# Kernel optimization log

Measured on AMD Instinct MI355X. Metric: run time of the kernel, lower is better.

## Reference

```python
import jax, jax.numpy as jnp
import numpy as np

N, K, D, H, DK, DV, E = 20000, 20, 128, 4, 32, 32, 128
HID = 4 * D


def _ln(x, g, b, eps=1e-5):
    m = x.mean(-1, keepdims=True)
    v = ((x - m) ** 2).mean(-1, keepdims=True)
    return (x - m) / jnp.sqrt(v + eps) * g + b


def setup_inputs() -> dict:
    key = jax.random.key(0)
    ks = jax.random.split(key, 24)
    inp = {
        "node_h_src": jax.random.normal(ks[0], (N, K, D), jnp.float32),
        "t": jax.random.uniform(ks[1], (N, K), jnp.float32),
        "t_now": jnp.ones((1,), jnp.float32),
        "edge_feat": jax.random.normal(ks[2], (N, K, E), jnp.float32),
        # time-encoding params (as in __init__)
        "basis_freq": jnp.asarray(1.0 / 10 ** np.linspace(0, 9, D), jnp.float32),
        "phase": jnp.zeros((D,), jnp.float32),
        # edge_fc
        "edge_fc_w": jax.random.normal(ks[3], (E, D), jnp.float32) * 0.05,
        "edge_fc_b": jnp.zeros((D,), jnp.float32),
        # QKV projections (stored as [in, out])
        "w_qs": jax.random.normal(ks[4], (D, H * DK), jnp.float32) * np.sqrt(2.0 / (D + DK)),
        "w_ks": jax.random.normal(ks[5], (D, H * DK), jnp.float32) * np.sqrt(2.0 / (D + DK)),
        "w_vs": jax.random.normal(ks[6], (D, H * DV), jnp.float32) * np.sqrt(2.0 / (D + DV)),
        "w_qs_src": jax.random.normal(ks[7], (D, H * DK), jnp.float32) * np.sqrt(2.0 / (D + DK)),
        # attn output fc
        "attn_fc_w": jax.random.normal(ks[8], (H * DV, D), jnp.float32) * 0.05,
        "attn_fc_b": jnp.zeros((D,), jnp.float32),
        "attn_ln_g": jnp.ones((D,), jnp.float32),
        "attn_ln_b": jnp.zeros((D,), jnp.float32),
        # positionwise FFN (Conv1d kernel 1 == linear)
        "ffn_w1": jax.random.normal(ks[9], (D, HID), jnp.float32) * 0.05,
        "ffn_b1": jnp.zeros((HID,), jnp.float32),
        "ffn_w2": jax.random.normal(ks[10], (HID, D), jnp.float32) * 0.05,
        "ffn_b2": jnp.zeros((D,), jnp.float32),
        "ffn_ln_g": jnp.ones((D,), jnp.float32),
        "ffn_ln_b": jnp.zeros((D,), jnp.float32),
        # fuse + output norm
        "fea2node_w": jax.random.normal(ks[11], (2 * D, D), jnp.float32) * 0.05,
        "fea2node_b": jnp.zeros((D,), jnp.float32),
        "out_ln_g": jnp.ones((D,), jnp.float32),
        "out_ln_b": jnp.zeros((D,), jnp.float32),
    }
    return inp


def reference(node_h_src, t, t_now, edge_feat, basis_freq, phase,
              edge_fc_w, edge_fc_b, w_qs, w_ks, w_vs, w_qs_src,
              attn_fc_w, attn_fc_b, attn_ln_g, attn_ln_b,
              ffn_w1, ffn_b1, ffn_w2, ffn_b2, ffn_ln_g, ffn_ln_b,
              fea2node_w, fea2node_b, out_ln_g, out_ln_b):
    gelu = lambda x: jax.nn.gelu(x, approximate=False)
    # message: temporal encoding + edge feature fusion
    t_enc = jnp.cos((t_now - t)[..., None] * basis_freq + phase)          # [N,K,D]
    z = node_h_src + gelu(edge_feat @ edge_fc_w + edge_fc_b) + t_enc      # [N,K,D]
    q = z @ w_qs                                                          # [N,K,H*DK]
    k = z @ w_ks
    v = z @ w_vs
    # reduce: self message replaces last slot. NOTE: original code uses
    # self_q for q, k AND v (w_ks_src/w_vs_src unused) -- reproduced faithfully.
    self_q = (z[:, -1, :] @ w_qs_src)[:, None, :]                         # [N,1,H*DK]
    q = jnp.concatenate([q[:, :-1, :], self_q], axis=1)
    k = jnp.concatenate([k[:, :-1, :], self_q], axis=1)
    v = jnp.concatenate([v[:, :-1, :], self_q], axis=1)
    qh = q.reshape(N, K, H, DK)
    kh = k.reshape(N, K, H, DK)
    vh = v.reshape(N, K, H, DV)
    attn = jnp.einsum("nqhd,nkhd->nhqk", qh, kh) / jnp.sqrt(jnp.float32(DK))
    attn = jax.nn.softmax(attn, axis=-1)
    out = jnp.einsum("nhqk,nkhd->nqhd", attn, vh).reshape(N, K, H * DV)
    out = out @ attn_fc_w + attn_fc_b
    x = _ln(out + z, attn_ln_g, attn_ln_b)                                # [N,K,D]
    # positionwise FFN with residual + LN
    ffn = jax.nn.relu(x @ ffn_w1 + ffn_b1) @ ffn_w2 + ffn_b2
    x = _ln(ffn + x, ffn_ln_g, ffn_ln_b)
    # fuse self slot with mean of neighbor slots
    neighborhood = x[:, :-1, :].mean(axis=1)                              # [N,D]
    fused = jnp.concatenate([x[:, -1, :], neighborhood], axis=-1)         # [N,2D]
    node_h = _ln(gelu(fused @ fea2node_w + fea2node_b) + node_h_src[:, -1, :],
                 out_ln_g, out_ln_b)
    return node_h
```

## Files before the change

kernel.cpp:

```cpp
#include <hip/hip_runtime.h>
#include <hip/hip_bf16.h>

#define N_NODES 20000
#define KK 20
#define DD 128
#define HH 4
#define DKK 32
#define EE 128
#define HIDD 512
#define RTOT (N_NODES * KK)

using bf16 = __hip_bfloat16;

typedef short s16x8 __attribute__((ext_vector_type(8)));
typedef float f32x4 __attribute__((ext_vector_type(4)));

__device__ __forceinline__ float geluf(float x) {
    return 0.5f * x * (1.0f + erff(x * 0.70710678118654752f));
}

__device__ __forceinline__ float wave_sum(float v) {
#pragma unroll
    for (int o = 32; o > 0; o >>= 1) v += __shfl_down(v, o);
    return __shfl(v, 0);
}

__global__ __launch_bounds__(256)
void k0_conv(const float* __restrict__ w1, const float* __restrict__ w2,
             bf16* __restrict__ w1t, bf16* __restrict__ w2t)
{
    const int id = blockIdx.x * 256 + threadIdx.x;
    if (id < HIDD * DD) {
        const int n = id / DD, k = id % DD;
        w1t[id] = __float2bfloat16(w1[k * HIDD + n]);
    } else {
        const int j = id - HIDD * DD;
        const int n = j / HIDD, k = j % HIDD;
        w2t[j] = __float2bfloat16(w2[k * DD + n]);
    }
}

__global__ __launch_bounds__(256)
void k0b_conv(const float* __restrict__ wq, const float* __restrict__ wk,
              const float* __restrict__ wv, const float* __restrict__ wqs,
              const float* __restrict__ afw, const float* __restrict__ ew,
              bf16* __restrict__ aw)
{
    const int id = blockIdx.x * 256 + threadIdx.x;
    const int m = id >> 14;
    const int r = id & 16383;
    const int n = r >> 7, k = r & 127;
    const float* src = (m == 0) ? wq : (m == 1) ? wk : (m == 2) ? wv
                     : (m == 3) ? wqs : (m == 4) ? afw : ew;
    aw[id] = __float2bfloat16(src[k * DD + n]);
}

__global__ __launch_bounds__(256)
void k1_msg(const float* __restrict__ nhs, const float* __restrict__ t,
            const float* __restrict__ t_now, const float* __restrict__ ef,
            const float* __restrict__ freq, const float* __restrict__ phase,
            const bf16* __restrict__ ewt, const float* __restrict__ eb,
            bf16* __restrict__ z)
{
    __shared__ bf16  efs[32][136];
    __shared__ float gs[32][132];
    __shared__ float ts[32];

    const int tid  = threadIdx.x;
    const int wv   = tid >> 6;
    const int lane = tid & 63;
    const int col  = lane & 15;
    const int quad = lane >> 4;
    const size_t base = (size_t)blockIdx.x * 32 * DD;

    {
        const float4* src = (const float4*)(ef + base);
#pragma unroll
        for (int it = 0; it < 4; it++) {
            const int i = tid + it * 256;
            const int r = i >> 5, c = (i & 31) * 4;
            const float4 v = src[i];
            bf16 tmp[4] = { __float2bfloat16(v.x), __float2bfloat16(v.y),
                            __float2bfloat16(v.z), __float2bfloat16(v.w) };
            *(uint2*)&efs[r][c] = *(const uint2*)tmp;
        }
    }
    if (tid < 32) ts[tid] = t[blockIdx.x * 32 + tid];
    __syncthreads();

    {
        f32x4 acc[2][2];
#pragma unroll
        for (int mt = 0; mt < 2; mt++)
#pragma unroll
            for (int nt = 0; nt < 2; nt++) acc[mt][nt] = (f32x4){0.f, 0.f, 0.f, 0.f};

#pragma unroll
        for (int kk = 0; kk < 4; kk++) {
            const int k0 = kk * 32 + quad * 8;
            const s16x8 a0 = *(const s16x8*)&efs[col][k0];
            const s16x8 a1 = *(const s16x8*)&efs[16 + col][k0];
#pragma unroll
            for (int nt = 0; nt < 2; nt++) {
                const int n = wv * 32 + nt * 16 + col;
                const s16x8 b = *(const s16x8*)&ewt[n * DD + k0];
                acc[0][nt] = __builtin_amdgcn_mfma_f32_16x16x32_bf16(a0, b, acc[0][nt], 0, 0, 0);
                acc[1][nt] = __builtin_amdgcn_mfma_f32_16x16x32_bf16(a1, b, acc[1][nt], 0, 0, 0);
            }
        }

#pragma unroll
        for (int mt = 0; mt < 2; mt++)
#pragma unroll
            for (int nt = 0; nt < 2; nt++) {
                const int n = wv * 32 + nt * 16 + col;
                const float bias = eb[n];
#pragma unroll
                for (int r = 0; r < 4; r++) {
                    const int row = mt * 16 + quad * 4 + r;
                    gs[row][n] = geluf(acc[mt][nt][r] + bias);
                }
            }
    }
    __syncthreads();

    {
        const float tn = t_now[0];
        const float4* nsrc = (const float4*)(nhs + base);
#pragma unroll
        for (int it = 0; it < 4; it++) {
            const int i = tid + it * 256;
            const int r = i >> 5, c = (i & 31) * 4;
            const float4 h  = nsrc[i];
            const float4 fq = *(const float4*)&freq[c];
            const float4 ph = *(const float4*)&phase[c];
            const float dt  = tn - ts[r];
            const float o0 = h.x + gs[r][c + 0] + __cosf(dt * fq.x + ph.x);
            const float o1 = h.y + gs[r][c + 1] + __cosf(dt * fq.y + ph.y);
            const float o2 = h.z + gs[r][c + 2] + __cosf(dt * fq.z + ph.z);
            const float o3 = h.w + gs[r][c + 3] + __cosf(dt * fq.w + ph.w);
            bf16 o[4] = { __float2bfloat16(o0), __float2bfloat16(o1),
                          __float2bfloat16(o2), __float2bfloat16(o3) };
            *(uint2*)&z[base + r * DD + c] = *(const uint2*)o;
        }
    }
}

__global__ __launch_bounds__(256, 4)
void k2_attn(bf16* __restrict__ zx, const bf16* __restrict__ aw,
             const float* __restrict__ afb,
             const float* __restrict__ lng, const float* __restrict__ lnb)
{
    __shared__ __align__(16) char smem[36352];
    bf16  (*zs)[136]    = (bf16  (*)[136])(smem);
    bf16  (*qb)[136]    = (bf16  (*)[136])(smem + 8704);
    bf16  (*kb)[136]    = (bf16  (*)[136])(smem + 17408);
    bf16  (*vT)[40]     = (bf16  (*)[40]) (smem + 26112);
    bf16  (*Pm)[32][40] = (bf16  (*)[32][40])(smem + 8704);
    bf16  (*obf)[136]   = (bf16  (*)[136])(smem + 8704);
    float (*us)[132]    = (float (*)[132])(smem + 8704);

    const int t    = threadIdx.x;
    const int wv4  = t >> 6;
    const int lane = t & 63;
    const int col  = lane & 15;
    const int quad = lane >> 4;
    const int node = blockIdx.x;
    bf16* zrow = zx + node * KK * DD;

    const uint4 z4 = make_uint4(0u, 0u, 0u, 0u);

    {
        const uint4* src = (const uint4*)zrow;
        for (int i = t; i < 320; i += 256) {
            const int r = i >> 4, c = (i & 15) * 8;
            *(uint4*)&zs[r][c] = src[i];
        }
        for (int i = t; i < 204; i += 256) {
            const int r = 20 + i / 17, c = (i % 17) * 8;
            *(uint4*)&zs[r][c] = z4;
        }
    }
    __syncthreads();

    {
        const bf16* Wm = aw + wv4 * (DD * DD);
        f32x4 acc[2][8];
#pragma unroll
        for (int mt = 0; mt < 2; mt++)
#pragma unroll
            for (int nt = 0; nt < 8; nt++) acc[mt][nt] = (f32x4){0.f, 0.f, 0.f, 0.f};

#pragma unroll
        for (int kk = 0; kk < 4; kk++) {
            const int k0 = kk * 32 + quad * 8;
            const s16x8 a0 = *(const s16x8*)&zs[col][k0];
            const s16x8 a1 = *(const s16x8*)&zs[16 + col][k0];
#pragma unroll
            for (int nt = 0; nt < 8; nt++) {
                const s16x8 b = *(const s16x8*)&Wm[(nt * 16 + col) * DD + k0];
                acc[0][nt] = __builtin_amdgcn_mfma_f32_16x16x32_bf16(a0, b, acc[0][nt], 0, 0, 0);
                acc[1][nt] = __builtin_amdgcn_mfma_f32_16x16x32_bf16(a1, b, acc[1][nt], 0, 0, 0);
            }
        }

        if (wv4 < 2) {
            bf16 (*dst)[136] = (wv4 == 0) ? qb : kb;
#pragma unroll
            for (int mt = 0; mt < 2; mt++)
#pragma unroll
                for (int nt = 0; nt < 8; nt++)
#pragma unroll
                    for (int r = 0; r < 4; r++) {
                        const int row = mt * 16 + quad * 4 + r;
                        if (row >= 19) continue;
                        dst[row][nt * 16 + col] = __float2bfloat16(acc[mt][nt][r]);
                    }
        } else if (wv4 == 2) {
#pragma unroll
            for (int mt = 0; mt < 2; mt++)
#pragma unroll
                for (int nt = 0; nt < 8; nt++)
#pragma unroll
                    for (int r = 0; r < 4; r++) {
                        const int row = mt * 16 + quad * 4 + r;
                        if (row == 19) continue;
                        vT[nt * 16 + col][row] = __float2bfloat16(acc[mt][nt][r]);
                    }
        } else if (quad == 0) {
#pragma unroll
            for (int nt = 0; nt < 8; nt++) {
                const int n = nt * 16 + col;
                const bf16 s = __float2bfloat16(acc[1][nt][3]);
                qb[19][n] = s; kb[19][n] = s; vT[n][19] = s;
            }
        }
    }
    __syncthreads();

    float p0[2][4], p1[2][4];
    {
        const int hb = wv4 * DKK;
        const int k0 = quad * 8;
        const s16x8 qa0 = *(const s16x8*)&qb[col][hb + k0];
        const s16x8 qa1 = *(const s16x8*)&qb[16 + col][hb + k0];
        const s16x8 kf0 = *(const s16x8*)&kb[col][hb + k0];
        const s16x8 kf1 = *(const s16x8*)&kb[16 + col][hb + k0];
        const f32x4 zero = (f32x4){0.f, 0.f, 0.f, 0.f};
        f32x4 sacc[2][2];
        sacc[0][0] = __builtin_amdgcn_mfma_f32_16x16x32_bf16(qa0, kf0, zero, 0, 0, 0);
        sacc[0][1] = __builtin_amdgcn_mfma_f32_16x16x32_bf16(qa0, kf1, zero, 0, 0, 0);
        sacc[1][0] = __builtin_amdgcn_mfma_f32_16x16x32_bf16(qa1, kf0, zero, 0, 0, 0);
        sacc[1][1] = __builtin_amdgcn_mfma_f32_16x16x32_bf16(qa1, kf1, zero, 0, 0, 0);

        const float scale = 0.17677669529663687f;
#pragma unroll
        for (int mt = 0; mt < 2; mt++)
#pragma unroll
            for (int r = 0; r < 4; r++) {
                const float s0 = sacc[mt][0][r] * scale;
                const float s1 = sacc[mt][1][r] * scale;
                float mx = fmaxf(s0, (col < 4) ? s1 : -1e30f);
#pragma unroll
                for (int o = 1; o < 16; o <<= 1) mx = fmaxf(mx, __shfl_xor(mx, o));
                const float e0 = __expf(s0 - mx);
                const float e1 = (col < 4) ? __expf(s1 - mx) : 0.f;
                float sm = e0 + e1;
#pragma unroll
                for (int o = 1; o < 16; o <<= 1) sm += __shfl_xor(sm, o);
                const float inv = 1.0f / sm;
                p0[mt][r] = e0 * inv;
                p1[mt][r] = e1 * inv;
            }
    }
    __syncthreads();

#pragma unroll
    for (int mt = 0; mt < 2; mt++)
#pragma unroll
        for (int r = 0; r < 4; r++) {
            const int i = mt * 16 + quad * 4 + r;
            Pm[wv4][i][col]      = __float2bfloat16(p0[mt][r]);
            Pm[wv4][i][16 + col] = __float2bfloat16(p1[mt][r]);
        }

    f32x4 oacc[2][2];
    {
        const int hb = wv4 * DKK;
        const int k0 = quad * 8;
        const s16x8 pa0 = *(const s16x8*)&Pm[wv4][col][k0];
        const s16x8 pa1 = *(const s16x8*)&Pm[wv4][16 + col][k0];
        const s16x8 vb0 = *(const s16x8*)&vT[hb + col][k0];
        const s16x8 vb1 = *(const s16x8*)&vT[hb + 16 + col][k0];
        const f32x4 zero = (f32x4){0.f, 0.f, 0.f, 0.f};
        oacc[0][0] = __builtin_amdgcn_mfma_f32_16x16x32_bf16(pa0, vb0, zero, 0, 0, 0);
        oacc[0][1] = __builtin_amdgcn_mfma_f32_16x16x32_bf16(pa0, vb1, zero, 0, 0, 0);
        oacc[1][0] = __builtin_amdgcn_mfma_f32_16x16x32_bf16(pa1, vb0, zero, 0, 0, 0);
        oacc[1][1] = __builtin_amdgcn_mfma_f32_16x16x32_bf16(pa1, vb1, zero, 0, 0, 0);
    }
    __syncthreads();

    {
        const int hb = wv4 * DKK;
#pragma unroll
        for (int mt = 0; mt < 2; mt++)
#pragma unroll
            for (int nt = 0; nt < 2; nt++)
#pragma unroll
                for (int r = 0; r < 4; r++)
                    obf[mt * 16 + quad * 4 + r][hb + nt * 16 + col] =
                        __float2bfloat16(oacc[mt][nt][r]);
    }
    __syncthreads();

    {
        const bf16* AF = aw + 4 * (DD * DD);
        f32x4 facc[2][2];
#pragma unroll
        for (int mt = 0; mt < 2; mt++)
#pragma unroll
            for (int nt = 0; nt < 2; nt++) facc[mt][nt] = (f32x4){0.f, 0.f, 0.f, 0.f};

#pragma unroll
        for (int kk = 0; kk < 4; kk++) {
            const int k0 = kk * 32 + quad * 8;
            const s16x8 a0 = *(const s16x8*)&obf[col][k0];
            const s16x8 a1 = *(const s16x8*)&obf[16 + col][k0];
#pragma unroll
            for (int nt = 0; nt < 2; nt++) {
                const int n = (wv4 * 2 + nt) * 16 + col;
                const s16x8 b = *(const s16x8*)&AF[n * DD + k0];
                facc[0][nt] = __builtin_amdgcn_mfma_f32_16x16x32_bf16(a0, b, facc[0][nt], 0, 0, 0);
                facc[1][nt] = __builtin_amdgcn_mfma_f32_16x16x32_bf16(a1, b, facc[1][nt], 0, 0, 0);
            }
        }
        __syncthreads();

#pragma unroll
        for (int mt = 0; mt < 2; mt++)
#pragma unroll
            for (int nt = 0; nt < 2; nt++) {
                const int n = (wv4 * 2 + nt) * 16 + col;
                const float bias = afb[n];
#pragma unroll
                for (int r = 0; r < 4; r++) {
                    const int i = mt * 16 + quad * 4 + r;
                    if (i >= 20) continue;
                    us[i][n] = facc[mt][nt][r] + bias + __bfloat162float(zs[i][n]);
                }
            }
    }
    __syncthreads();

    for (int i = wv4; i < KK; i += 4) {
        const float a0 = us[i][lane], a1 = us[i][lane + 64];
        const float s  = wave_sum(a0 + a1);
        const float sq = wave_sum(a0 * a0 + a1 * a1);
        const float mean = s * (1.0f / DD);
        const float var  = sq * (1.0f / DD) - mean * mean;
        const float inv  = rsqrtf(var + 1e-5f);
        zrow[i * DD + lane]      = __float2bfloat16((a0 - mean) * inv * lng[lane] + lnb[lane]);
        zrow[i * DD + lane + 64] = __float2bfloat16((a1 - mean) * inv * lng[lane + 64] + lnb[lane + 64]);
    }
}

#define XPAD (DD + 8)
#define HPAD (HIDD + 8)

__global__ __launch_bounds__(256)
void k3_ffn(bf16* __restrict__ zx,
            const bf16* __restrict__ w1t, const float* __restrict__ b1,
            const bf16* __restrict__ w2t, const float* __restrict__ b2,
            const float* __restrict__ lng, const float* __restrict__ lnb)
{
    __shared__ bf16 xs[32][XPAD];
    __shared__ bf16 h1[32][HPAD];

    const int t    = threadIdx.x;
    const int wv   = t >> 6;
    const int lane = t & 63;
    const int col  = lane & 15;
    const int quad = lane >> 4;
    const int base = blockIdx.x * 32 * DD;

    {
        const uint4* src = (const uint4*)(zx + base);
#pragma unroll
        for (int it = 0; it < 2; it++) {
            const int i = t + it * 256;
            const int r = i >> 4, c = (i & 15) * 8;
            *(uint4*)&xs[r][c] = src[i];
        }
    }
    __syncthreads();

    {
        f32x4 acc[2][8];
#pragma unroll
        for (int mt = 0; mt < 2; mt++)
#pragma unroll
            for (int nt = 0; nt < 8; nt++) acc[mt][nt] = (f32x4){0.f, 0.f, 0.f, 0.f};

#pragma unroll
        for (int kk = 0; kk < 4; kk++) {
            const int k0 = kk * 32 + quad * 8;
            const s16x8 a0 = *(const s16x8*)&xs[col][k0];
            const s16x8 a1 = *(const s16x8*)&xs[16 + col][k0];
#pragma unroll
            for (int nt = 0; nt < 8; nt++) {
                const int n = wv * 128 + nt * 16 + col;
                const s16x8 b = *(const s16x8*)&w1t[n * DD + k0];
                acc[0][nt] = __builtin_amdgcn_mfma_f32_16x16x32_bf16(a0, b, acc[0][nt], 0, 0, 0);
                acc[1][nt] = __builtin_amdgcn_mfma_f32_16x16x32_bf16(a1, b, acc[1][nt], 0, 0, 0);
            }
        }
#pragma unroll
        for (int nt = 0; nt < 8; nt++) {
            const int n = wv * 128 + nt * 16 + col;
            const float bias = b1[n];
#pragma unroll
            for (int r = 0; r < 4; r++) {
                const int row = quad * 4 + r;
                h1[row][n]      = __float2bfloat16(fmaxf(acc[0][nt][r] + bias, 0.f));
                h1[16 + row][n] = __float2bfloat16(fmaxf(acc[1][nt][r] + bias, 0.f));
            }
        }
    }
    __syncthreads();

    {
        f32x4 acc[2][2];
#pragma unroll
        for (int mt = 0; mt < 2; mt++)
#pragma unroll
            for (int nt = 0; nt < 2; nt++) acc[mt][nt] = (f32x4){0.f, 0.f, 0.f, 0.f};

#pragma unroll 4
        for (int kk = 0; kk < 16; kk++) {
            const int k0 = kk * 32 + quad * 8;
            const s16x8 a0 = *(const s16x8*)&h1[col][k0];
            const s16x8 a1 = *(const s16x8*)&h1[16 + col][k0];
#pragma unroll
            for (int nt = 0; nt < 2; nt++) {
                const int n = wv * 32 + nt * 16 + col;
                const s16x8 b = *(const s16x8*)&w2t[n * HIDD + k0];
                acc[0][nt] = __builtin_amdgcn_mfma_f32_16x16x32_bf16(a0, b, acc[0][nt], 0, 0, 0);
                acc[1][nt] = __builtin_amdgcn_mfma_f32_16x16x32_bf16(a1, b, acc[1][nt], 0, 0, 0);
            }
        }
        __syncthreads();

        float* u = (float*)&h1[0][0];
#pragma unroll
        for (int mt = 0; mt < 2; mt++)
#pragma unroll
            for (int nt = 0; nt < 2; nt++) {
                const int n = wv * 32 + nt * 16 + col;
                const float bias = b2[n];
#pragma unroll
                for (int r = 0; r < 4; r++) {
                    const int row = mt * 16 + quad * 4 + r;
                    u[row * DD + n] = acc[mt][nt][r] + bias + __bfloat162float(xs[row][n]);
                }
            }
    }
    __syncthreads();

    {
        const float* u = (const float*)&h1[0][0];
        for (int r = wv; r < 32; r += 4) {
            const float a0 = u[r * DD + lane], a1 = u[r * DD + lane + 64];
            const float s  = wave_sum(a0 + a1);
            const float sq = wave_sum(a0 * a0 + a1 * a1);
            const float mean = s * (1.0f / DD);
            const float var  = sq * (1.0f / DD) - mean * mean;
            const float inv  = rsqrtf(var + 1e-5f);
            zx[base + r * DD + lane]      = __float2bfloat16((a0 - mean) * inv * lng[lane] + lnb[lane]);
            zx[base + r * DD + lane + 64] = __float2bfloat16((a1 - mean) * inv * lng[lane + 64] + lnb[lane + 64]);
        }
    }
}

__global__ __launch_bounds__(128)
void k4_fuse(const bf16* __restrict__ zx, const float* __restrict__ nhs,
             const float* __restrict__ fw, const float* __restrict__ fb,
             const float* __restrict__ lng, const float* __restrict__ lnb,
             float* __restrict__ out)
{
    __shared__ float f[2 * DD];
    __shared__ float red[4];
    const int d = threadIdx.x;
    const int node = blockIdx.x;
    const bf16* xr = zx + node * KK * DD;

    float nb = 0.f;
#pragma unroll
    for (int i = 0; i < KK - 1; i++) nb += __bfloat162float(xr[i * DD + d]);
    f[d] = __bfloat162float(xr[(KK - 1) * DD + d]);
    f[DD + d] = nb * (1.0f / (KK - 1));
    __syncthreads();

    float a = fb[d];
#pragma unroll 4
    for (int c = 0; c < 2 * DD; c++) a += f[c] * fw[c * DD + d];
    const float y = geluf(a) + nhs[(node * KK + KK - 1) * DD + d];

    float s = y, sq = y * y;
#pragma unroll
    for (int o = 32; o > 0; o >>= 1) {
        s += __shfl_down(s, o);
        sq += __shfl_down(sq, o);
    }
    const int wid = d >> 6, lane = d & 63;
    if (lane == 0) { red[wid] = s; red[2 + wid] = sq; }
    __syncthreads();
    const float ts = red[0] + red[1], tsq = red[2] + red[3];
    const float mean = ts * (1.0f / DD);
    const float var = tsq * (1.0f / DD) - mean * mean;
    const float inv = rsqrtf(var + 1e-5f);
    out[node * DD + d] = (y - mean) * inv * lng[d] + lnb[d];
}

extern "C" void kernel_launch(void* const* d_in, const int* in_sizes, int n_in,
                              void* d_out, int out_size, void* d_ws, size_t ws_size,
                              hipStream_t stream)
{
    const float* nhs   = (const float*)d_in[0];
    const float* t     = (const float*)d_in[1];
    const float* tnow  = (const float*)d_in[2];
    const float* ef    = (const float*)d_in[3];
    const float* freq  = (const float*)d_in[4];
    const float* phase = (const float*)d_in[5];
    const float* ew    = (const float*)d_in[6];
    const float* eb    = (const float*)d_in[7];
    const float* wq    = (const float*)d_in[8];
    const float* wk    = (const float*)d_in[9];
    const float* wv    = (const float*)d_in[10];
    const float* wqs   = (const float*)d_in[11];
    const float* afw   = (const float*)d_in[12];
    const float* afb   = (const float*)d_in[13];
    const float* alng  = (const float*)d_in[14];
    const float* alnb  = (const float*)d_in[15];
    const float* w1    = (const float*)d_in[16];
    const float* b1    = (const float*)d_in[17];
    const float* w2    = (const float*)d_in[18];
    const float* b2    = (const float*)d_in[19];
    const float* flng  = (const float*)d_in[20];
    const float* flnb  = (const float*)d_in[21];
    const float* fw    = (const float*)d_in[22];
    const float* fb    = (const float*)d_in[23];
    const float* olng  = (const float*)d_in[24];
    const float* olnb  = (const float*)d_in[25];
    float* out = (float*)d_out;

    bf16* zx  = (bf16*)d_ws;
    bf16* w1t = (bf16*)((char*)d_ws + (size_t)RTOT * DD * 2);
    bf16* w2t = w1t + HIDD * DD;
    bf16* aw  = w2t + DD * HIDD;
    bf16* ewt = aw + 5 * DD * DD;

    k0_conv<<<dim3(2 * HIDD * DD / 256), dim3(256), 0, stream>>>(w1, w2, w1t, w2t);
    k0b_conv<<<dim3(6 * DD * DD / 256), dim3(256), 0, stream>>>(wq, wk, wv, wqs, afw, ew, aw);
    k1_msg<<<dim3(RTOT / 32), dim3(256), 0, stream>>>(nhs, t, tnow, ef, freq, phase, ewt, eb, zx);
    k2_attn<<<dim3(N_NODES), dim3(256), 0, stream>>>(zx, aw, afb, alng, alnb);
    k3_ffn<<<dim3(RTOT / 32), dim3(256), 0, stream>>>(zx, w1t, b1, w2t, b2, flng, flnb);
    k4_fuse<<<dim3(N_NODES), dim3(128), 0, stream>>>(zx, nhs, fw, fb, olng, olnb, out);
}
```

Baseline: 1.367 ms.

## Fuse message, attention, FFN and fuse stages into one per-node kernel

Merges the four per-row/per-node kernels (edge message, attention, FFN, fuse/output norm) into a single kernel that handles one node per block, keeping the 20-row activation tile in shared memory throughout. This removes the bf16 intermediate round-trips through global memory between stages and the extra launches. The FFN hidden layer is processed in two 256-wide chunks to fit shared memory, and fea2node weights are pre-converted to bf16. In exchange, the 32-row MFMA tiles now carry 12 padding rows per block, and the longer kernel is more complex with heavy shared-memory aliasing.

```diff
diff --git a/kernel.cpp b/kernel.cpp
--- a/kernel.cpp
+++ b/kernel.cpp
@@ -44,141 +44,124 @@
 void k0b_conv(const float* __restrict__ wq, const float* __restrict__ wk,
               const float* __restrict__ wv, const float* __restrict__ wqs,
               const float* __restrict__ afw, const float* __restrict__ ew,
-              bf16* __restrict__ aw)
+              const float* __restrict__ fw, bf16* __restrict__ aw)
 {
     const int id = blockIdx.x * 256 + threadIdx.x;
     const int m = id >> 14;
     const int r = id & 16383;
-    const int n = r >> 7, k = r & 127;
-    const float* src = (m == 0) ? wq : (m == 1) ? wk : (m == 2) ? wv
-                     : (m == 3) ? wqs : (m == 4) ? afw : ew;
-    aw[id] = __float2bfloat16(src[k * DD + n]);
+    if (m < 6) {
+        const int n = r >> 7, k = r & 127;
+        const float* src = (m == 0) ? wq : (m == 1) ? wk : (m == 2) ? wv
+                         : (m == 3) ? wqs : (m == 4) ? afw : ew;
+        aw[id] = __float2bfloat16(src[k * DD + n]);
+    } else {
+        aw[id] = __float2bfloat16(fw[(m - 6) * 16384 + r]);
+    }
 }
 
-__global__ __launch_bounds__(256)
-void k1_msg(const float* __restrict__ nhs, const float* __restrict__ t,
+#define O_NHF   5440
+#define O_KB    5440
+#define O_FUSED 10880
+#define O_PART  11904
+#define O_RED   12928
+#define O_TS    16000
+#define O_ZS    16096
+#define O_VT    21536
+#define O_XB    21536
+#define SMEM_SZ 31776
+
+__global__ __launch_bounds__(256, 5)
+void k_node(const float* __restrict__ nhs, const float* __restrict__ t,
             const float* __restrict__ t_now, const float* __restrict__ ef,
             const float* __restrict__ freq, const float* __restrict__ phase,
-            const bf16* __restrict__ ewt, const float* __restrict__ eb,
-            bf16* __restrict__ z)
+            const float* __restrict__ eb,
+            const bf16* __restrict__ aw, const float* __restrict__ afb,
+            const float* __restrict__ alng, const float* __restrict__ alnb,
+            const bf16* __restrict__ w1t, const float* __restrict__ b1,
+            const bf16* __restrict__ w2t, const float* __restrict__ b2,
+            const float* __restrict__ flng, const float* __restrict__ flnb,
+            const float* __restrict__ fb,
+            const float* __restrict__ olng, const float* __restrict__ olnb,
+            float* __restrict__ out)
 {
-    __shared__ bf16  efs[32][136];
-    __shared__ float gs[32][132];
-    __shared__ float ts[32];
+    __shared__ __align__(16) char smem[SMEM_SZ];
+    bf16  (*efb)[136]   = (bf16  (*)[136])(smem);
+    bf16  (*qb)[136]    = (bf16  (*)[136])(smem);
+    bf16  (*Pm)[32][40] = (bf16  (*)[32][40])(smem);
+    bf16  (*obf)[136]   = (bf16  (*)[136])(smem);
+    float (*us)[132]    = (float (*)[132])(smem);
+    bf16  (*h1)[264]    = (bf16  (*)[264])(smem);
+    float (*nhf)[132]   = (float (*)[132])(smem + O_NHF);
+    bf16  (*kb)[136]    = (bf16  (*)[136])(smem + O_KB);
+    float *fused        = (float*)(smem + O_FUSED);
+    float (*part)[128]  = (float (*)[128])(smem + O_PART);
+    float *red          = (float*)(smem + O_RED);
+    float *ts           = (float*)(smem + O_TS);
+    bf16  (*zs)[136]    = (bf16  (*)[136])(smem + O_ZS);
+    bf16  (*vT)[40]     = (bf16  (*)[40]) (smem + O_VT);
+    bf16  (*xb)[136]    = (bf16  (*)[136])(smem + O_XB);
 
     const int tid  = threadIdx.x;
-    const int wv   = tid >> 6;
+    const int wv4  = tid >> 6;
     const int lane = tid & 63;
     const int col  = lane & 15;
     const int quad = lane >> 4;
-    const size_t base = (size_t)blockIdx.x * 32 * DD;
-
-    {
-        const float4* src = (const float4*)(ef + base);
-#pragma unroll
-        for (int it = 0; it < 4; it++) {
-            const int i = tid + it * 256;
+    const int node = blockIdx.x;
+    const size_t base = (size_t)node * KK * DD;
+    const bf16* ewt = aw + 5 * (DD * DD);
+    const bf16* fwb = aw + 6 * (DD * DD);
+    const f32x4 fzero = (f32x4){0.f, 0.f, 0.f, 0.f};
+
+    {
+        const float4* esrc = (const float4*)(ef + base);
+        const float4* nsrc = (const float4*)(nhs + base);
+        for (int i = tid; i < 640; i += 256) {
             const int r = i >> 5, c = (i & 31) * 4;
-            const float4 v = src[i];
+            const float4 v = esrc[i];
             bf16 tmp[4] = { __float2bfloat16(v.x), __float2bfloat16(v.y),
                             __float2bfloat16(v.z), __float2bfloat16(v.w) };
-            *(uint2*)&efs[r][c] = *(const uint2*)tmp;
-        }
-    }
-    if (tid < 32) ts[tid] = t[blockIdx.x * 32 + tid];
-    __syncthreads();
-
-    {
-        f32x4 acc[2][2];
+            *(uint2*)&efb[r][c] = *(const uint2*)tmp;
+            *(float4*)&nhf[r][c] = nsrc[i];
+        }
+        if (tid < KK) ts[tid] = t[node * KK + tid];
+    }
+    __syncthreads();
+
+    {
+        f32x4 eacc[2][2];
 #pragma unroll
         for (int mt = 0; mt < 2; mt++)
 #pragma unroll
-            for (int nt = 0; nt < 2; nt++) acc[mt][nt] = (f32x4){0.f, 0.f, 0.f, 0.f};
-
+            for (int nt = 0; nt < 2; nt++) eacc[mt][nt] = fzero;
 #pragma unroll
         for (int kk = 0; kk < 4; kk++) {
             const int k0 = kk * 32 + quad * 8;
-            const s16x8 a0 = *(const s16x8*)&efs[col][k0];
-            const s16x8 a1 = *(const s16x8*)&efs[16 + col][k0];
+            const s16x8 a0 = *(const s16x8*)&efb[col][k0];
+            const s16x8 a1 = *(const s16x8*)&efb[16 + col][k0];
 #pragma unroll
             for (int nt = 0; nt < 2; nt++) {
-                const int n = wv * 32 + nt * 16 + col;
+                const int n = wv4 * 32 + nt * 16 + col;
                 const s16x8 b = *(const s16x8*)&ewt[n * DD + k0];
-                acc[0][nt] = __builtin_amdgcn_mfma_f32_16x16x32_bf16(a0, b, acc[0][nt], 0, 0, 0);
-                acc[1][nt] = __builtin_amdgcn_mfma_f32_16x16x32_bf16(a1, b, acc[1][nt], 0, 0, 0);
-            }
-        }
-
-#pragma unroll
-        for (int mt = 0; mt < 2; mt++)
-#pragma unroll
-            for (int nt = 0; nt < 2; nt++) {
-                const int n = wv * 32 + nt * 16 + col;
-                const float bias = eb[n];
+                eacc[0][nt] = __builtin_amdgcn_mfma_f32_16x16x32_bf16(a0, b, eacc[0][nt], 0, 0, 0);
+                eacc[1][nt] = __builtin_amdgcn_mfma_f32_16x16x32_bf16(a1, b, eacc[1][nt], 0, 0, 0);
+            }
+        }
+        const float tn = t_now[0];
+#pragma unroll
+        for (int nt = 0; nt < 2; nt++) {
+            const int n = wv4 * 32 + nt * 16 + col;
+            const float bias = eb[n], fq = freq[n], ph = phase[n];
+#pragma unroll
+            for (int mt = 0; mt < 2; mt++)
 #pragma unroll
                 for (int r = 0; r < 4; r++) {
                     const int row = mt * 16 + quad * 4 + r;
-                    gs[row][n] = geluf(acc[mt][nt][r] + bias);
+                    if (row < KK) {
+                        const float zz = nhf[row][n] + geluf(eacc[mt][nt][r] + bias)
+                                       + __cosf((tn - ts[row]) * fq + ph);
+                        zs[row][n] = __float2bfloat16(zz);
+                    }
                 }
-            }
-    }
-    __syncthreads();
-
-    {
-        const float tn = t_now[0];
-        const float4* nsrc = (const float4*)(nhs + base);
-#pragma unroll
-        for (int it = 0; it < 4; it++) {
-            const int i = tid + it * 256;
-            const int r = i >> 5, c = (i & 31) * 4;
-            const float4 h  = nsrc[i];
-            const float4 fq = *(const float4*)&freq[c];
-            const float4 ph = *(const float4*)&phase[c];
-            const float dt  = tn - ts[r];
-            const float o0 = h.x + gs[r][c + 0] + __cosf(dt * fq.x + ph.x);
-            const float o1 = h.y + gs[r][c + 1] + __cosf(dt * fq.y + ph.y);
-            const float o2 = h.z + gs[r][c + 2] + __cosf(dt * fq.z + ph.z);
-            const float o3 = h.w + gs[r][c + 3] + __cosf(dt * fq.w + ph.w);
-            bf16 o[4] = { __float2bfloat16(o0), __float2bfloat16(o1),
-                          __float2bfloat16(o2), __float2bfloat16(o3) };
-            *(uint2*)&z[base + r * DD + c] = *(const uint2*)o;
-        }
-    }
-}
-
-__global__ __launch_bounds__(256, 4)
-void k2_attn(bf16* __restrict__ zx, const bf16* __restrict__ aw,
-             const float* __restrict__ afb,
-             const float* __restrict__ lng, const float* __restrict__ lnb)
-{
-    __shared__ __align__(16) char smem[36352];
-    bf16  (*zs)[136]    = (bf16  (*)[136])(smem);
-    bf16  (*qb)[136]    = (bf16  (*)[136])(smem + 8704);
-    bf16  (*kb)[136]    = (bf16  (*)[136])(smem + 17408);
-    bf16  (*vT)[40]     = (bf16  (*)[40]) (smem + 26112);
-    bf16  (*Pm)[32][40] = (bf16  (*)[32][40])(smem + 8704);
-    bf16  (*obf)[136]   = (bf16  (*)[136])(smem + 8704);
-    float (*us)[132]    = (float (*)[132])(smem + 8704);
-
-    const int t    = threadIdx.x;
-    const int wv4  = t >> 6;
-    const int lane = t & 63;
-    const int col  = lane & 15;
-    const int quad = lane >> 4;
-    const int node = blockIdx.x;
-    bf16* zrow = zx + node * KK * DD;
-
-    const uint4 z4 = make_uint4(0u, 0u, 0u, 0u);
-
-    {
-        const uint4* src = (const uint4*)zrow;
-        for (int i = t; i < 320; i += 256) {
-            const int r = i >> 4, c = (i & 15) * 8;
-            *(uint4*)&zs[r][c] = src[i];
-        }
-        for (int i = t; i < 204; i += 256) {
-            const int r = 20 + i / 17, c = (i % 17) * 8;
-            *(uint4*)&zs[r][c] = z4;
         }
     }
     __syncthreads();
@@ -189,8 +172,7 @@
 #pragma unroll
         for (int mt = 0; mt < 2; mt++)
 #pragma unroll
-            for (int nt = 0; nt < 8; nt++) acc[mt][nt] = (f32x4){0.f, 0.f, 0.f, 0.f};
-
+            for (int nt = 0; nt < 8; nt++) acc[mt][nt] = fzero;
 #pragma unroll
         for (int kk = 0; kk < 4; kk++) {
             const int k0 = kk * 32 + quad * 8;
@@ -203,7 +185,6 @@
                 acc[1][nt] = __builtin_amdgcn_mfma_f32_16x16x32_bf16(a1, b, acc[1][nt], 0, 0, 0);
             }
         }
-
         if (wv4 < 2) {
             bf16 (*dst)[136] = (wv4 == 0) ? qb : kb;
 #pragma unroll
@@ -225,7 +206,8 @@
                     for (int r = 0; r < 4; r++) {
                         const int row = mt * 16 + quad * 4 + r;
                         if (row == 19) continue;
-                        vT[nt * 16 + col][row] = __float2bfloat16(acc[mt][nt][r]);
+                        vT[nt * 16 + col][row] =
+                            (row < 19) ? __float2bfloat16(acc[mt][nt][r]) : __float2bfloat16(0.f);
                     }
         } else if (quad == 0) {
 #pragma unroll
@@ -246,12 +228,11 @@
         const s16x8 qa1 = *(const s16x8*)&qb[16 + col][hb + k0];
         const s16x8 kf0 = *(const s16x8*)&kb[col][hb + k0];
         const s16x8 kf1 = *(const s16x8*)&kb[16 + col][hb + k0];
-        const f32x4 zero = (f32x4){0.f, 0.f, 0.f, 0.f};
         f32x4 sacc[2][2];
-        sacc[0][0] = __builtin_amdgcn_mfma_f32_16x16x32_bf16(qa0, kf0, zero, 0, 0, 0);
-        sacc[0][1] = __builtin_amdgcn_mfma_f32_16x16x32_bf16(qa0, kf1, zero, 0, 0, 0);
-        sacc[1][0] = __builtin_amdgcn_mfma_f32_16x16x32_bf16(qa1, kf0, zero, 0, 0, 0);
-        sacc[1][1] = __builtin_amdgcn_mfma_f32_16x16x32_bf16(qa1, kf1, zero, 0, 0, 0);
+        sacc[0][0] = __builtin_amdgcn_mfma_f32_16x16x32_bf16(qa0, kf0, fzero, 0, 0, 0);
+        sacc[0][1] = __builtin_amdgcn_mfma_f32_16x16x32_bf16(qa0, kf1, fzero, 0, 0, 0);
+        sacc[1][0] = __builtin_amdgcn_mfma_f32_16x16x32_bf16(qa1, kf0, fzero, 0, 0, 0);
+        sacc[1][1] = __builtin_amdgcn_mfma_f32_16x16x32_bf16(qa1, kf1, fzero, 0, 0, 0);
 
         const float scale = 0.17677669529663687f;
 #pragma unroll
@@ -283,7 +264,6 @@
             Pm[wv4][i][col]      = __float2bfloat16(p0[mt][r]);
             Pm[wv4][i][16 + col] = __float2bfloat16(p1[mt][r]);
         }
-
     f32x4 oacc[2][2];
     {
         const int hb = wv4 * DKK;
@@ -292,11 +272,10 @@
         const s16x8 pa1 = *(const s16x8*)&Pm[wv4][16 + col][k0];
         const s16x8 vb0 = *(const s16x8*)&vT[hb + col][k0];
         const s16x8 vb1 = *(const s16x8*)&vT[hb + 16 + col][k0];
-        const f32x4 zero = (f32x4){0.f, 0.f, 0.f, 0.f};
-        oacc[0][0] = __builtin_amdgcn_mfma_f32_16x16x32_bf16(pa0, vb0, zero, 0, 0, 0);
-        oacc[0][1] = __builtin_amdgcn_mfma_f32_16x16x32_bf16(pa0, vb1, zero, 0, 0, 0);
-        oacc[1][0] = __builtin_amdgcn_mfma_f32_16x16x32_bf16(pa1, vb0, zero, 0, 0, 0);
-        oacc[1][1] = __builtin_amdgcn_mfma_f32_16x16x32_bf16(pa1, vb1, zero, 0, 0, 0);
+        oacc[0][0] = __builtin_amdgcn_mfma_f32_16x16x32_bf16(pa0, vb0, fzero, 0, 0, 0);
+        oacc[0][1] = __builtin_amdgcn_mfma_f32_16x16x32_bf16(pa0, vb1, fzero, 0, 0, 0);
+        oacc[1][0] = __builtin_amdgcn_mfma_f32_16x16x32_bf16(pa1, vb0, fzero, 0, 0, 0);
+        oacc[1][1] = __builtin_amdgcn_mfma_f32_16x16x32_bf16(pa1, vb1, fzero, 0, 0, 0);
     }
     __syncthreads();
 
@@ -319,8 +298,7 @@
 #pragma unroll
         for (int mt = 0; mt < 2; mt++)
 #pragma unroll
-            for (int nt = 0; nt < 2; nt++) facc[mt][nt] = (f32x4){0.f, 0.f, 0.f, 0.f};
-
+            for (int nt = 0; nt < 2; nt++) facc[mt][nt] = fzero;
 #pragma unroll
         for (int kk = 0; kk < 4; kk++) {
             const int k0 = kk * 32 + quad * 8;
@@ -345,7 +323,7 @@
 #pragma unroll
                 for (int r = 0; r < 4; r++) {
                     const int i = mt * 16 + quad * 4 + r;
-                    if (i >= 20) continue;
+                    if (i >= KK) continue;
                     us[i][n] = facc[mt][nt][r] + bias + __bfloat162float(zs[i][n]);
                 }
             }
@@ -359,166 +337,142 @@
         const float mean = s * (1.0f / DD);
         const float var  = sq * (1.0f / DD) - mean * mean;
         const float inv  = rsqrtf(var + 1e-5f);
-        zrow[i * DD + lane]      = __float2bfloat16((a0 - mean) * inv * lng[lane] + lnb[lane]);
-        zrow[i * DD + lane + 64] = __float2bfloat16((a1 - mean) * inv * lng[lane + 64] + lnb[lane + 64]);
-    }
-}
-
-#define XPAD (DD + 8)
-#define HPAD (HIDD + 8)
-
-__global__ __launch_bounds__(256)
-void k3_ffn(bf16* __restrict__ zx,
-            const bf16* __restrict__ w1t, const float* __restrict__ b1,
-            const bf16* __restrict__ w2t, const float* __restrict__ b2,
-            const float* __restrict__ lng, const float* __restrict__ lnb)
-{
-    __shared__ bf16 xs[32][XPAD];
-    __shared__ bf16 h1[32][HPAD];
-
-    const int t    = threadIdx.x;
-    const int wv   = t >> 6;
-    const int lane = t & 63;
-    const int col  = lane & 15;
-    const int quad = lane >> 4;
-    const int base = blockIdx.x * 32 * DD;
-
-    {
-        const uint4* src = (const uint4*)(zx + base);
-#pragma unroll
-        for (int it = 0; it < 2; it++) {
-            const int i = t + it * 256;
-            const int r = i >> 4, c = (i & 15) * 8;
-            *(uint4*)&xs[r][c] = src[i];
-        }
-    }
-    __syncthreads();
-
-    {
-        f32x4 acc[2][8];
-#pragma unroll
-        for (int mt = 0; mt < 2; mt++)
-#pragma unroll
-            for (int nt = 0; nt < 8; nt++) acc[mt][nt] = (f32x4){0.f, 0.f, 0.f, 0.f};
-
-#pragma unroll
-        for (int kk = 0; kk < 4; kk++) {
-            const int k0 = kk * 32 + quad * 8;
-            const s16x8 a0 = *(const s16x8*)&xs[col][k0];
-            const s16x8 a1 = *(const s16x8*)&xs[16 + col][k0];
-#pragma unroll
-            for (int nt = 0; nt < 8; nt++) {
-                const int n = wv * 128 + nt * 16 + col;
-                const s16x8 b = *(const s16x8*)&w1t[n * DD + k0];
-                acc[0][nt] = __builtin_amdgcn_mfma_f32_16x16x32_bf16(a0, b, acc[0][nt], 0, 0, 0);
-                acc[1][nt] = __builtin_amdgcn_mfma_f32_16x16x32_bf16(a1, b, acc[1][nt], 0, 0, 0);
-            }
-        }
-#pragma unroll
-        for (int nt = 0; nt < 8; nt++) {
-            const int n = wv * 128 + nt * 16 + col;
-            const float bias = b1[n];
+        xb[i][lane]      = __float2bfloat16((a0 - mean) * inv * alng[lane] + alnb[lane]);
+        xb[i][lane + 64] = __float2bfloat16((a1 - mean) * inv * alng[lane + 64] + alnb[lane + 64]);
+    }
+    __syncthreads();
+
+    f32x4 acc2[2][2];
+#pragma unroll
+    for (int mt = 0; mt < 2; mt++)
+#pragma unroll
+        for (int nt = 0; nt < 2; nt++) acc2[mt][nt] = fzero;
+
+#pragma unroll
+    for (int ch = 0; ch < 2; ch++) {
+        {
+            f32x4 acc[2][4];
+#pragma unroll
+            for (int mt = 0; mt < 2; mt++)
+#pragma unroll
+                for (int nt = 0; nt < 4; nt++) acc[mt][nt] = fzero;
+#pragma unroll
+            for (int kk = 0; kk < 4; kk++) {
+                const int k0 = kk * 32 + quad * 8;
+                const s16x8 a0 = *(const s16x8*)&xb[col][k0];
+                const s16x8 a1 = *(const s16x8*)&xb[16 + col][k0];
+#pragma unroll
+                for (int nt = 0; nt < 4; nt++) {
+                    const int n = ch * 256 + wv4 * 64 + nt * 16 + col;
+                    const s16x8 b = *(const s16x8*)&w1t[n * DD + k0];
+                    acc[0][nt] = __builtin_amdgcn_mfma_f32_16x16x32_bf16(a0, b, acc[0][nt], 0, 0, 0);
+                    acc[1][nt] = __builtin_amdgcn_mfma_f32_16x16x32_bf16(a1, b, acc[1][nt], 0, 0, 0);
+                }
+            }
+#pragma unroll
+            for (int nt = 0; nt < 4; nt++) {
+                const int nl = wv4 * 64 + nt * 16 + col;
+                const float bias = b1[ch * 256 + nl];
+#pragma unroll
+                for (int mt = 0; mt < 2; mt++)
+#pragma unroll
+                    for (int r = 0; r < 4; r++) {
+                        const int row = mt * 16 + quad * 4 + r;
+                        if (row < KK)
+                            h1[row][nl] = __float2bfloat16(fmaxf(acc[mt][nt][r] + bias, 0.f));
+                    }
+            }
+        }
+        __syncthreads();
+
+        {
+#pragma unroll
+            for (int kk = 0; kk < 8; kk++) {
+                const int k0l = kk * 32 + quad * 8;
+                const s16x8 a0 = *(const s16x8*)&h1[col][k0l];
+                const s16x8 a1 = *(const s16x8*)&h1[16 + col][k0l];
+#pragma unroll
+                for (int nt = 0; nt < 2; nt++) {
+                    const int n = wv4 * 32 + nt * 16 + col;
+                    const s16x8 b = *(const s16x8*)&w2t[n * HIDD + ch * 256 + k0l];
+                    acc2[0][nt] = __builtin_amdgcn_mfma_f32_16x16x32_bf16(a0, b, acc2[0][nt], 0, 0, 0);
+                    acc2[1][nt] = __builtin_amdgcn_mfma_f32_16x16x32_bf16(a1, b, acc2[1][nt], 0, 0, 0);
+                }
+            }
+        }
+        __syncthreads();
+    }
+
+#pragma unroll
+    for (int mt = 0; mt < 2; mt++)
+#pragma unroll
+        for (int nt = 0; nt < 2; nt++) {
+            const int n = wv4 * 32 + nt * 16 + col;
+            const float bias = b2[n];
 #pragma unroll
             for (int r = 0; r < 4; r++) {
-                const int row = quad * 4 + r;
-                h1[row][n]      = __float2bfloat16(fmaxf(acc[0][nt][r] + bias, 0.f));
-                h1[16 + row][n] = __float2bfloat16(fmaxf(acc[1][nt][r] + bias, 0.f));
-            }
-        }
-    }
-    __syncthreads();
-
-    {
-        f32x4 acc[2][2];
-#pragma unroll
-        for (int mt = 0; mt < 2; mt++)
-#pragma unroll
-            for (int nt = 0; nt < 2; nt++) acc[mt][nt] = (f32x4){0.f, 0.f, 0.f, 0.f};
-
-#pragma unroll 4
-        for (int kk = 0; kk < 16; kk++) {
-            const int k0 = kk * 32 + quad * 8;
-            const s16x8 a0 = *(const s16x8*)&h1[col][k0];
-            const s16x8 a1 = *(const s16x8*)&h1[16 + col][k0];
-#pragma unroll
-            for (int nt = 0; nt < 2; nt++) {
-                const int n = wv * 32 + nt * 16 + col;
-                const s16x8 b = *(const s16x8*)&w2t[n * HIDD + k0];
-                acc[0][nt] = __builtin_amdgcn_mfma_f32_16x16x32_bf16(a0, b, acc[0][nt], 0, 0, 0);
-                acc[1][nt] = __builtin_amdgcn_mfma_f32_16x16x32_bf16(a1, b, acc[1][nt], 0, 0, 0);
-            }
-        }
-        __syncthreads();
-
-        float* u = (float*)&h1[0][0];
-#pragma unroll
-        for (int mt = 0; mt < 2; mt++)
-#pragma unroll
-            for (int nt = 0; nt < 2; nt++) {
-                const int n = wv * 32 + nt * 16 + col;
-                const float bias = b2[n];
-#pragma unroll
-                for (int r = 0; r < 4; r++) {
-                    const int row = mt * 16 + quad * 4 + r;
-                    u[row * DD + n] = acc[mt][nt][r] + bias + __bfloat162float(xs[row][n]);
-                }
-            }
-    }
-    __syncthreads();
-
-    {
-        const float* u = (const float*)&h1[0][0];
-        for (int r = wv; r < 32; r += 4) {
-            const float a0 = u[r * DD + lane], a1 = u[r * DD + lane + 64];
-            const float s  = wave_sum(a0 + a1);
-            const float sq = wave_sum(a0 * a0 + a1 * a1);
-            const float mean = s * (1.0f / DD);
-            const float var  = sq * (1.0f / DD) - mean * mean;
-            const float inv  = rsqrtf(var + 1e-5f);
-            zx[base + r * DD + lane]      = __float2bfloat16((a0 - mean) * inv * lng[lane] + lnb[lane]);
-            zx[base + r * DD + lane + 64] = __float2bfloat16((a1 - mean) * inv * lng[lane + 64] + lnb[lane + 64]);
-        }
-    }
-}
-
-__global__ __launch_bounds__(128)
-void k4_fuse(const bf16* __restrict__ zx, const float* __restrict__ nhs,
-             const float* __restrict__ fw, const float* __restrict__ fb,
-             const float* __restrict__ lng, const float* __restrict__ lnb,
-             float* __restrict__ out)
-{
-    __shared__ float f[2 * DD];
-    __shared__ float red[4];
-    const int d = threadIdx.x;
-    const int node = blockIdx.x;
-    const bf16* xr = zx + node * KK * DD;
-
-    float nb = 0.f;
-#pragma unroll
-    for (int i = 0; i < KK - 1; i++) nb += __bfloat162float(xr[i * DD + d]);
-    f[d] = __bfloat162float(xr[(KK - 1) * DD + d]);
-    f[DD + d] = nb * (1.0f / (KK - 1));
-    __syncthreads();
-
-    float a = fb[d];
-#pragma unroll 4
-    for (int c = 0; c < 2 * DD; c++) a += f[c] * fw[c * DD + d];
-    const float y = geluf(a) + nhs[(node * KK + KK - 1) * DD + d];
-
-    float s = y, sq = y * y;
-#pragma unroll
-    for (int o = 32; o > 0; o >>= 1) {
-        s += __shfl_down(s, o);
-        sq += __shfl_down(sq, o);
-    }
-    const int wid = d >> 6, lane = d & 63;
-    if (lane == 0) { red[wid] = s; red[2 + wid] = sq; }
-    __syncthreads();
-    const float ts = red[0] + red[1], tsq = red[2] + red[3];
-    const float mean = ts * (1.0f / DD);
-    const float var = tsq * (1.0f / DD) - mean * mean;
-    const float inv = rsqrtf(var + 1e-5f);
-    out[node * DD + d] = (y - mean) * inv * lng[d] + lnb[d];
+                const int i = mt * 16 + quad * 4 + r;
+                if (i >= KK) continue;
+                us[i][n] = acc2[mt][nt][r] + bias + __bfloat162float(xb[i][n]);
+            }
+        }
+    __syncthreads();
+
+    for (int i = wv4; i < KK; i += 4) {
+        const float a0 = us[i][lane], a1 = us[i][lane + 64];
+        const float s  = wave_sum(a0 + a1);
+        const float sq = wave_sum(a0 * a0 + a1 * a1);
+        const float mean = s * (1.0f / DD);
+        const float var  = sq * (1.0f / DD) - mean * mean;
+        const float inv  = rsqrtf(var + 1e-5f);
+        us[i][lane]      = (a0 - mean) * inv * flng[lane] + flnb[lane];
+        us[i][lane + 64] = (a1 - mean) * inv * flng[lane + 64] + flnb[lane + 64];
+    }
+    __syncthreads();
+
+    if (tid < DD) {
+        fused[tid] = us[19][tid];
+    } else {
+        const int d = tid - DD;
+        float nb = 0.f;
+#pragma unroll
+        for (int i = 0; i < KK - 1; i++) nb += us[i][d];
+        fused[DD + d] = nb * (1.0f / (KK - 1));
+    }
+    __syncthreads();
+
+    {
+        const int d = tid & 127, hb2 = tid >> 7;
+        float a = 0.f;
+#pragma unroll 8
+        for (int ci = 0; ci < 128; ci++) {
+            const int c = hb2 * 128 + ci;
+            a += fused[c] * __bfloat162float(fwb[c * DD + d]);
+        }
+        part[hb2][d] = a;
+    }
+    __syncthreads();
+
+    float y = 0.f;
+    if (tid < DD) {
+        y = geluf(part[0][tid] + part[1][tid] + fb[tid]) + nhs[base + (KK - 1) * DD + tid];
+        float s = y, sq = y * y;
+#pragma unroll
+        for (int o = 32; o > 0; o >>= 1) {
+            s += __shfl_down(s, o);
+            sq += __shfl_down(sq, o);
+        }
+        const int wid = tid >> 6, ln = tid & 63;
+        if (ln == 0) { red[wid] = s; red[2 + wid] = sq; }
+    }
+    __syncthreads();
+    if (tid < DD) {
+        const float tsm = red[0] + red[1], tsq = red[2] + red[3];
+        const float mean = tsm * (1.0f / DD);
+        const float var  = tsq * (1.0f / DD) - mean * mean;
+        const float inv  = rsqrtf(var + 1e-5f);
+        out[node * DD + tid] = (y - mean) * inv * olng[tid] + olnb[tid];
+    }
 }
 
 extern "C" void kernel_launch(void* const* d_in, const int* in_sizes, int n_in,
@@ -553,16 +507,13 @@
     const float* olnb  = (const float*)d_in[25];
     float* out = (float*)d_out;
 
-    bf16* zx  = (bf16*)d_ws;
-    bf16* w1t = (bf16*)((char*)d_ws + (size_t)RTOT * DD * 2);
+    bf16* w1t = (bf16*)d_ws;
     bf16* w2t = w1t + HIDD * DD;
     bf16* aw  = w2t + DD * HIDD;
-    bf16* ewt = aw + 5 * DD * DD;
 
     k0_conv<<<dim3(2 * HIDD * DD / 256), dim3(256), 0, stream>>>(w1, w2, w1t, w2t);
-    k0b_conv<<<dim3(6 * DD * DD / 256), dim3(256), 0, stream>>>(wq, wk, wv, wqs, afw, ew, aw);
-    k1_msg<<<dim3(RTOT / 32), dim3(256), 0, stream>>>(nhs, t, tnow, ef, freq, phase, ewt, eb, zx);
-    k2_attn<<<dim3(N_NODES), dim3(256), 0, stream>>>(zx, aw, afb, alng, alnb);
-    k3_ffn<<<dim3(RTOT / 32), dim3(256), 0, stream>>>(zx, w1t, b1, w2t, b2, flng, flnb);
-    k4_fuse<<<dim3(N_NODES), dim3(128), 0, stream>>>(zx, nhs, fw, fb, olng, olnb, out);
+    k0b_conv<<<dim3(8 * DD * DD / 256), dim3(256), 0, stream>>>(wq, wk, wv, wqs, afw, ew, fw, aw);
+    k_node<<<dim3(N_NODES), dim3(256), 0, stream>>>(
+        nhs, t, tnow, ef, freq, phase, eb, aw, afb, alng, alnb,
+        w1t, b1, w2t, b2, flng, flnb, fb, olng, olnb, out);
 }
```

New measurement: 1.708 ms. 1.25x slower.
